# Performance work log

Measured on AMD Instinct MI355X. Metric: run time of the kernel, lower is better.

Reference implementation:

```python
import jax, jax.numpy as jnp
import numpy as np

N = 50000      # nodes
E = 800000     # edges (before self-loops)
IN = 128       # in_dim
OUT = 128      # out_dim
H = 4          # heads
C = OUT // H   # per-head channels
G = 64         # number of graphs in batch
NEG_SLOPE = 0.2
GN_EPS = 1e-5


def setup_inputs() -> dict:
    key = jax.random.key(0)
    ks = jax.random.split(key, 6)
    x = jax.random.normal(ks[0], (N, IN), dtype=jnp.float32)
    edge_index = jax.random.randint(ks[1], (2, E), 0, N, dtype=jnp.int32)
    batch = jnp.sort(jax.random.randint(ks[2], (N,), 0, G, dtype=jnp.int32))
    # glorot-ish init for GATv2 params
    s = float(np.sqrt(6.0 / (IN + H * C)))
    Wl = jax.random.uniform(ks[3], (IN, H * C), jnp.float32, -s, s)  # source (lin_l)
    Wr = jax.random.uniform(ks[4], (IN, H * C), jnp.float32, -s, s)  # target (lin_r)
    sa = float(np.sqrt(6.0 / (C + 1)))
    att = jax.random.uniform(ks[5], (H, C), jnp.float32, -sa, sa)
    bias_conv = jnp.zeros((H * C,), jnp.float32)
    gn_weight = jnp.ones((OUT,), jnp.float32)
    gn_bias = jnp.zeros((OUT,), jnp.float32)
    gn_mean_scale = jnp.ones((OUT,), jnp.float32)
    return {"x": x, "edge_index": edge_index, "batch": batch,
            "Wl": Wl, "Wr": Wr, "att": att, "bias_conv": bias_conv,
            "gn_weight": gn_weight, "gn_bias": gn_bias, "gn_mean_scale": gn_mean_scale}


def reference(x, edge_index, batch, Wl, Wr, att, bias_conv, gn_weight, gn_bias, gn_mean_scale):
    n = x.shape[0]
    # --- GATv2Conv (eval: dropout off), add_self_loops=True ---
    loop = jnp.arange(n, dtype=edge_index.dtype)
    src = jnp.concatenate([edge_index[0], loop])  # source j
    dst = jnp.concatenate([edge_index[1], loop])  # target i
    xl = (x @ Wl).reshape(n, H, C)  # source-side features
    xr = (x @ Wr).reshape(n, H, C)  # target-side features
    m = xl[src] + xr[dst]                               # [E', H, C]
    e = jax.nn.leaky_relu(m, NEG_SLOPE)
    logits = jnp.einsum('ehc,hc->eh', e, att)           # [E', H]
    # segment softmax over destination nodes
    amax = jax.ops.segment_max(logits, dst, num_segments=n)   # [N, H]
    ex = jnp.exp(logits - amax[dst])
    denom = jax.ops.segment_sum(ex, dst, num_segments=n)      # [N, H]
    alpha = ex / (denom[dst] + 1e-16)
    out = jax.ops.segment_sum(alpha[:, :, None] * xl[src], dst, num_segments=n)  # [N, H, C]
    out = out.reshape(n, H * C) + bias_conv
    # --- GraphNorm: (x - a*mean_g) / sqrt(var_g + eps) * w + b ---
    ones = jnp.ones((n, 1), out.dtype)
    cnt = jnp.maximum(jax.ops.segment_sum(ones, batch, num_segments=G), 1.0)  # [G, 1]
    mean = jax.ops.segment_sum(out, batch, num_segments=G) / cnt             # [G, OUT]
    out_c = out - mean[batch] * gn_mean_scale
    var = jax.ops.segment_sum(out_c * out_c, batch, num_segments=G) / cnt    # [G, OUT]
    y = out_c / jnp.sqrt(var[batch] + GN_EPS) * gn_weight + gn_bias
    # --- ELU ---
    return jax.nn.elu(y)
```

## Files before the change

### kernel.cpp

```cpp
#include <hip/hip_runtime.h>
#include <math.h>

#define HH 4
#define GG 64
#define CHUNK 64
#define BDST 16
#define BSH  4
#define SLOT 768
#define NPT  16
#define HWORDS 3328
constexpr float NEG_SLOPE = 0.2f;
constexpr float GN_EPS = 1e-5f;

typedef __attribute__((ext_vector_type(8))) short bf16x8;
typedef __attribute__((ext_vector_type(4))) float f32x4;

__device__ __forceinline__ unsigned short f2bf_rne(float f) {
  unsigned u = __float_as_uint(f);
  u += 0x7fffu + ((u >> 16) & 1u);
  return (unsigned short)(u >> 16);
}

__global__ __launch_bounds__(256) void wpack(
    const float* __restrict__ Wl, const float* __restrict__ Wr,
    unsigned short* __restrict__ Bfrag) {
  int tid = blockIdx.x * 256 + threadIdx.x;
  int f = tid >> 6, l = tid & 63;
  int m = f >> 5;
  int t = (f >> 2) & 7;
  int ks = f & 3;
  int col = t * 16 + (l & 15);
  int k0 = ks * 32 + (l >> 4) * 8;
  const float* W = m ? Wr : Wl;
  unsigned short* dst = Bfrag + ((size_t)f * 64 + l) * 8;
  #pragma unroll
  for (int j = 0; j < 8; ++j)
    dst[j] = f2bf_rne(W[(k0 + j) * 128 + col]);
}

__global__ __launch_bounds__(256) void gemm_mfma(
    const float* __restrict__ x, const unsigned short* __restrict__ Bfrag,
    unsigned short* __restrict__ xlb, float* __restrict__ xr, int n) {
  const int wave = (blockIdx.x * 256 + threadIdx.x) >> 6;
  if (wave * 16 >= n) return;
  const int l = threadIdx.x & 63;
  const int arow = min(wave * 16 + (l & 15), n - 1);
  const float4* xrow = reinterpret_cast<const float4*>(x + (size_t)arow * 128);

  bf16x8 a[4];
  #pragma unroll
  for (int ks = 0; ks < 4; ++ks) {
    float4 lo = xrow[ks * 8 + (l >> 4) * 2];
    float4 hi = xrow[ks * 8 + (l >> 4) * 2 + 1];
    bf16x8 v;
    v[0] = (short)f2bf_rne(lo.x); v[1] = (short)f2bf_rne(lo.y);
    v[2] = (short)f2bf_rne(lo.z); v[3] = (short)f2bf_rne(lo.w);
    v[4] = (short)f2bf_rne(hi.x); v[5] = (short)f2bf_rne(hi.y);
    v[6] = (short)f2bf_rne(hi.z); v[7] = (short)f2bf_rne(hi.w);
    a[ks] = v;
  }

  const int r0 = wave * 16 + (l >> 4) * 4;
  const int cb = l & 15;
  #pragma unroll
  for (int t = 0; t < 8; ++t) {
    f32x4 acc = {0.f, 0.f, 0.f, 0.f};
    #pragma unroll
    for (int ks = 0; ks < 4; ++ks) {
      const bf16x8* bp = reinterpret_cast<const bf16x8*>(
          Bfrag + ((size_t)((0 * 8 + t) * 4 + ks) * 64 + l) * 8);
      acc = __builtin_amdgcn_mfma_f32_16x16x32_bf16(a[ks], *bp, acc, 0, 0, 0);
    }
    #pragma unroll
    for (int j = 0; j < 4; ++j) {
      int r = r0 + j;
      if (r < n) xlb[(size_t)r * 128 + t * 16 + cb] = f2bf_rne(acc[j]);
    }
  }
  #pragma unroll
  for (int t = 0; t < 8; ++t) {
    f32x4 acc = {0.f, 0.f, 0.f, 0.f};
    #pragma unroll
    for (int ks = 0; ks < 4; ++ks) {
      const bf16x8* bp = reinterpret_cast<const bf16x8*>(
          Bfrag + ((size_t)((1 * 8 + t) * 4 + ks) * 64 + l) * 8);
      acc = __builtin_amdgcn_mfma_f32_16x16x32_bf16(a[ks], *bp, acc, 0, 0, 0);
    }
    #pragma unroll
    for (int j = 0; j < 4; ++j) {
      int r = r0 + j;
      if (r < n) xr[(size_t)r * 128 + t * 16 + cb] = acc[j];
    }
  }
}

__global__ __launch_bounds__(256) void bucket_scatter(
    const int* __restrict__ ei, int* __restrict__ gcur,
    int* __restrict__ ebuf, int E, int E2, int nbk) {
  __shared__ int hist[HWORDS];
  const int t = threadIdx.x;
  for (int i = t; i < HWORDS; i += 256) hist[i] = 0;
  __syncthreads();
  unsigned wcache[NPT];
  const int base = blockIdx.x * (256 * NPT);
  #pragma unroll
  for (int i = 0; i < NPT; ++i) {
    int e = base + i * 256 + t;
    unsigned w = 0xFFFFFFFFu;
    if (e < E2) {
      int src, dst;
      if (e < E) { src = ei[e]; dst = ei[E + e]; }
      else       { src = e - E; dst = e - E; }
      w = ((unsigned)(dst >> BSH) << 20) | ((unsigned)(dst & (BDST - 1)) << 16)
          | (unsigned)src;
      atomicAdd(&hist[dst >> BSH], 1);
    }
    wcache[i] = w;
  }
  __syncthreads();
  for (int b = t; b < nbk; b += 256) {
    int c = hist[b];
    if (c) hist[b] = atomicAdd(&gcur[b], c);
  }
  __syncthreads();
  #pragma unroll
  for (int i = 0; i < NPT; ++i) {
    unsigned w = wcache[i];
    if (w == 0xFFFFFFFFu) continue;
    int b = w >> 20;
    int pos = atomicAdd(&hist[b], 1);
    if (pos < SLOT) ebuf[b * SLOT + pos] = (int)(w & 0xFFFFF);
  }
}

__global__ __launch_bounds__(256) void fused_aggr(
    const int* __restrict__ gcur, const int* __restrict__ ebuf,
    const unsigned char* __restrict__ xb,
    const float* __restrict__ xr, const float* __restrict__ att,
    float* __restrict__ out, int n) {
  __shared__ int eraw[SLOT];
  __shared__ int elist[SLOT + 16];
  __shared__ int ldeg[BDST];
  __shared__ int lrow[BDST + 1];
  __shared__ int lcur[BDST];
  const int b = blockIdx.x;
  const int t = threadIdx.x;
  const int cnt = min(gcur[b], SLOT);
  if (t < BDST) ldeg[t] = 0;
  __syncthreads();
  for (int i = t; i < cnt; i += 256) {
    int w = ebuf[b * SLOT + i];
    eraw[i] = w;
    atomicAdd(&ldeg[(w >> 16) & (BDST - 1)], 1);
  }
  __syncthreads();
  if (t < BDST) {
    int v = ldeg[t];
    int incl = v;
    #pragma unroll
    for (int d = 1; d < BDST; d <<= 1) {
      int u = __shfl_up(incl, d);
      if (t >= d) incl += u;
    }
    lrow[t] = incl - v;
    lcur[t] = incl - v;
    if (t == BDST - 1) lrow[BDST] = incl;
  }
  __syncthreads();
  for (int i = t; i < cnt; i += 256) {
    int w = eraw[i];
    int pos = atomicAdd(&lcur[(w >> 16) & (BDST - 1)], 1);
    elist[pos] = (w & 0xFFFF) << 8;
  }
  if (t < 16) elist[cnt + t] = 0;
  __syncthreads();

  const int wv = t >> 6, lane = t & 63;
  const int q = lane & 31, hf = lane >> 5;
  const float4 at4 = *reinterpret_cast<const float4*>(att + q * 4);

  #define LDE(st) (*reinterpret_cast<const uint2*>( \
      xb + (size_t)(unsigned)ep[2 * (st) + hf] + q * 8))
  #define STEP(V, ebase) { \
    float x0 = __uint_as_float((V).x << 16); \
    float x1 = __uint_as_float((V).x & 0xffff0000u); \
    float x2 = __uint_as_float((V).y << 16); \
    float x3 = __uint_as_float((V).y & 0xffff0000u); \
    float t0 = x0 + xr4.x; t0 = fmaxf(t0, NEG_SLOPE * t0); \
    float t1 = x1 + xr4.y; t1 = fmaxf(t1, NEG_SLOPE * t1); \
    float t2 = x2 + xr4.z; t2 = fmaxf(t2, NEG_SLOPE * t2); \
    float t3 = x3 + xr4.w; t3 = fmaxf(t3, NEG_SLOPE * t3); \
    float p = fmaf(t3, at4.w, fmaf(t2, at4.z, fmaf(t1, at4.y, t0 * at4.x))); \
    p += __shfl_xor(p, 1); \
    p += __shfl_xor(p, 2); \
    p += __shfl_xor(p, 4); \
    float w = ((ebase) + hf < deg) ? __expf(p) : 0.f; \
    s += w; \
    a0 = fmaf(w, x0, a0); a1 = fmaf(w, x1, a1); \
    a2 = fmaf(w, x2, a2); a3 = fmaf(w, x3, a3); }

  for (int j = 0; j < 4; ++j) {
    const int ldst = wv * 4 + j;
    const int node = b * BDST + ldst;
    if (node >= n) break;
    const float4 xr4 = *reinterpret_cast<const float4*>(xr + (size_t)node * 128 + q * 4);
    const int k0 = lrow[ldst];
    const int deg = lrow[ldst + 1] - k0;
    const int* ep = elist + k0;

    uint2 V0 = LDE(0), V1 = LDE(1), V2 = LDE(2), V3 = LDE(3);
    float s = 0.f, a0 = 0.f, a1 = 0.f, a2 = 0.f, a3 = 0.f;
    const int S = (deg + 1) >> 1;
    for (int i = 0; i < S; i += 2) {
      STEP(V0, 2 * i)
      STEP(V1, 2 * i + 2)
      V0 = V2; V1 = V3;
      if (2 * i + 8 < deg)  V2 = LDE(i + 4);
      if (2 * i + 10 < deg) V3 = LDE(i + 5);
    }
    s  += __shfl_xor(s, 32);
    a0 += __shfl_xor(a0, 32);
    a1 += __shfl_xor(a1, 32);
    a2 += __shfl_xor(a2, 32);
    a3 += __shfl_xor(a3, 32);
    float inv = 1.f / (s + 1e-16f);
    if (hf == 0)
      *reinterpret_cast<float4*>(out + (size_t)node * 128 + q * 4) =
          make_float4(a0 * inv, a1 * inv, a2 * inv, a3 * inv);
  }
  #undef STEP
  #undef LDE
}

__global__ __launch_bounds__(128) void gn_stats(
    const float* __restrict__ out, const float* __restrict__ bias,
    const int* __restrict__ batch, float* __restrict__ gsum,
    float* __restrict__ gsumsq, int* __restrict__ gcnt, int n) {
  const int c = threadIdx.x;
  const int n0 = blockIdx.x * CHUNK;
  const int n1 = min(n0 + CHUNK, n);
  const float bc = bias[c];
  float bsum = 0.f, bsq = 0.f;
  int cnt = 0;
  int curg = batch[n0];
  for (int nid = n0; nid < n1; ++nid) {
    int g = batch[nid];
    if (g != curg) {
      atomicAdd(&gsum[curg * 128 + c], bsum);
      atomicAdd(&gsumsq[curg * 128 + c], bsq);
      if (c == 0) atomicAdd(&gcnt[curg], cnt);
      bsum = 0.f; bsq = 0.f; cnt = 0; curg = g;
    }
    float v = out[(size_t)nid * 128 + c] + bc;
    bsum += v; bsq += v * v; ++cnt;
  }
  atomicAdd(&gsum[curg * 128 + c], bsum);
  atomicAdd(&gsumsq[curg * 128 + c], bsq);
  if (c == 0) atomicAdd(&gcnt[curg], cnt);
}

__global__ __launch_bounds__(128) void gn_prep(
    const float* __restrict__ gsum, const float* __restrict__ gsumsq,
    const int* __restrict__ gcnt, const float* __restrict__ bias,
    const float* __restrict__ msc, const float* __restrict__ w,
    const float* __restrict__ b, float* __restrict__ K, float* __restrict__ S) {
  int g = blockIdx.x, c = threadIdx.x;
  float cnt = (float)max(gcnt[g], 1);
  float mean = gsum[g * 128 + c] / cnt;
  float a = msc[c];
  float var = gsumsq[g * 128 + c] / cnt - mean * mean * (2.f * a - a * a);
  float k = rsqrtf(var + GN_EPS) * w[c];
  K[g * 128 + c] = k;
  S[g * 128 + c] = (bias[c] - mean * a) * k + b[c];
}

__global__ __launch_bounds__(256) void gn_norm(
    float* __restrict__ out, const int* __restrict__ batch,
    const float* __restrict__ K, const float* __restrict__ S, int n) {
  long long i = (long long)blockIdx.x * 256 + threadIdx.x;
  if (i >= (long long)n * 128) return;
  int nid = (int)(i >> 7), c = (int)(i & 127);
  int g = batch[nid];
  float val = fmaf(out[i], K[g * 128 + c], S[g * 128 + c]);
  out[i] = (val > 0.f) ? val : (__expf(val) - 1.f);
}

extern "C" void kernel_launch(void* const* d_in, const int* in_sizes, int n_in,
                              void* d_out, int out_size, void* d_ws, size_t ws_size,
                              hipStream_t stream) {
  const float* x    = (const float*)d_in[0];
  const int*   ei   = (const int*)d_in[1];
  const int*   batch= (const int*)d_in[2];
  const float* Wl   = (const float*)d_in[3];
  const float* Wr   = (const float*)d_in[4];
  const float* att  = (const float*)d_in[5];
  const float* bias = (const float*)d_in[6];
  const float* gw   = (const float*)d_in[7];
  const float* gb   = (const float*)d_in[8];
  const float* gms  = (const float*)d_in[9];
  float* out = (float*)d_out;

  const int n  = in_sizes[0] / 128;
  const int E  = in_sizes[1] / 2;
  const int E2 = E + n;
  const int NBK = (n + BDST - 1) / BDST;

  char* ws = (char*)d_ws;
  size_t off = 0;
  int*   gcur    = (int*)(ws + off); off += (size_t)((NBK + 63) & ~63) * 4;
  int*   gcnt    = (int*)(ws + off); off += GG * 4;
  float* gsum    = (float*)(ws + off); off += GG * 128 * 4;
  float* gsumsq  = (float*)(ws + off); off += GG * 128 * 4;
  size_t zero_bytes = off;
  int*   ebuf    = (int*)(ws + off); off += (size_t)NBK * SLOT * 4;
  unsigned short* xlb = (unsigned short*)(ws + off); off += (size_t)n * 128 * 2;
  float* xr      = (float*)(ws + off); off += (size_t)n * 128 * 4;
  unsigned short* Bfrag = (unsigned short*)(ws + off); off += 64 * 64 * 8 * 2;
  float* gK      = (float*)(ws + off); off += GG * 128 * 4;
  float* gS      = (float*)(ws + off); off += GG * 128 * 4;

  hipMemsetAsync(ws, 0, zero_bytes, stream);

  bucket_scatter<<<(E2 + 256 * NPT - 1) / (256 * NPT), 256, 0, stream>>>(
      ei, gcur, ebuf, E, E2, NBK);

  wpack<<<16, 256, 0, stream>>>(Wl, Wr, (unsigned short*)Bfrag);
  {
    int waves = (n + 15) / 16;
    int blocks = (waves * 64 + 255) / 256;
    gemm_mfma<<<blocks, 256, 0, stream>>>(x, Bfrag, xlb, xr, n);
  }

  fused_aggr<<<NBK, 256, 0, stream>>>(gcur, ebuf, (const unsigned char*)xlb,
                                      xr, att, out, n);

  gn_stats<<<(n + CHUNK - 1) / CHUNK, 128, 0, stream>>>(out, bias, batch, gsum, gsumsq, gcnt, n);
  gn_prep<<<GG, 128, 0, stream>>>(gsum, gsumsq, gcnt, bias, gms, gw, gb, gK, gS);

  long long t_nm = (long long)n * 128;
  gn_norm<<<(int)((t_nm + 255) / 256), 256, 0, stream>>>(out, batch, gK, gS, n);
}
```

Before: 130.8 us.

## Merge bucket scatter with GEMM, widen aggregation lanes, vectorize GraphNorm apply

Merges the edge bucket-scatter kernel and the MFMA projection GEMM into one launch, with blocks split by index, so the two independent phases share a grid and one launch is dropped. The aggregation kernel now has each lane handle 8 channels (16-byte loads) and processes 4 edges per wave step instead of 2. The per-head reduction needs fewer shuffles, but more registers are held per lane. The GraphNorm apply kernel now uses float4 loads and stores. The merged kernel's blocks all reserve the histogram shared memory, including the GEMM blocks, which may lower their occupancy.

New measurement: 116.9 us. 1.12x faster.

```diff
diff --git a/kernel.cpp b/kernel.cpp
--- a/kernel.cpp
+++ b/kernel.cpp
@@ -38,12 +38,51 @@
     dst[j] = f2bf_rne(W[(k0 + j) * 128 + col]);
 }
 
-__global__ __launch_bounds__(256) void gemm_mfma(
+__global__ __launch_bounds__(256) void prep_merged(
+    const int* __restrict__ ei, int* __restrict__ gcur, int* __restrict__ ebuf,
+    int E, int E2, int nbk, int SB,
     const float* __restrict__ x, const unsigned short* __restrict__ Bfrag,
     unsigned short* __restrict__ xlb, float* __restrict__ xr, int n) {
-  const int wave = (blockIdx.x * 256 + threadIdx.x) >> 6;
+  __shared__ int hist[HWORDS];
+  const int t = threadIdx.x;
+  if ((int)blockIdx.x < SB) {
+    for (int i = t; i < HWORDS; i += 256) hist[i] = 0;
+    __syncthreads();
+    unsigned wcache[NPT];
+    const int base = blockIdx.x * (256 * NPT);
+    #pragma unroll
+    for (int i = 0; i < NPT; ++i) {
+      int e = base + i * 256 + t;
+      unsigned w = 0xFFFFFFFFu;
+      if (e < E2) {
+        int src, dst;
+        if (e < E) { src = ei[e]; dst = ei[E + e]; }
+        else       { src = e - E; dst = e - E; }
+        w = ((unsigned)(dst >> BSH) << 20) | ((unsigned)(dst & (BDST - 1)) << 16)
+            | (unsigned)src;
+        atomicAdd(&hist[dst >> BSH], 1);
+      }
+      wcache[i] = w;
+    }
+    __syncthreads();
+    for (int b = t; b < nbk; b += 256) {
+      int c = hist[b];
+      if (c) hist[b] = atomicAdd(&gcur[b], c);
+    }
+    __syncthreads();
+    #pragma unroll
+    for (int i = 0; i < NPT; ++i) {
+      unsigned w = wcache[i];
+      if (w == 0xFFFFFFFFu) continue;
+      int b = w >> 20;
+      int pos = atomicAdd(&hist[b], 1);
+      if (pos < SLOT) ebuf[b * SLOT + pos] = (int)(w & 0xFFFFF);
+    }
+    return;
+  }
+  const int wave = ((blockIdx.x - SB) * 256 + t) >> 6;
   if (wave * 16 >= n) return;
-  const int l = threadIdx.x & 63;
+  const int l = t & 63;
   const int arow = min(wave * 16 + (l & 15), n - 1);
   const float4* xrow = reinterpret_cast<const float4*>(x + (size_t)arow * 128);
 
@@ -63,73 +102,34 @@
   const int r0 = wave * 16 + (l >> 4) * 4;
   const int cb = l & 15;
   #pragma unroll
-  for (int t = 0; t < 8; ++t) {
+  for (int tt = 0; tt < 8; ++tt) {
     f32x4 acc = {0.f, 0.f, 0.f, 0.f};
     #pragma unroll
     for (int ks = 0; ks < 4; ++ks) {
       const bf16x8* bp = reinterpret_cast<const bf16x8*>(
-          Bfrag + ((size_t)((0 * 8 + t) * 4 + ks) * 64 + l) * 8);
+          Bfrag + ((size_t)((0 * 8 + tt) * 4 + ks) * 64 + l) * 8);
       acc = __builtin_amdgcn_mfma_f32_16x16x32_bf16(a[ks], *bp, acc, 0, 0, 0);
     }
     #pragma unroll
     for (int j = 0; j < 4; ++j) {
       int r = r0 + j;
-      if (r < n) xlb[(size_t)r * 128 + t * 16 + cb] = f2bf_rne(acc[j]);
+      if (r < n) xlb[(size_t)r * 128 + tt * 16 + cb] = f2bf_rne(acc[j]);
     }
   }
   #pragma unroll
-  for (int t = 0; t < 8; ++t) {
+  for (int tt = 0; tt < 8; ++tt) {
     f32x4 acc = {0.f, 0.f, 0.f, 0.f};
     #pragma unroll
     for (int ks = 0; ks < 4; ++ks) {
       const bf16x8* bp = reinterpret_cast<const bf16x8*>(
-          Bfrag + ((size_t)((1 * 8 + t) * 4 + ks) * 64 + l) * 8);
+          Bfrag + ((size_t)((1 * 8 + tt) * 4 + ks) * 64 + l) * 8);
       acc = __builtin_amdgcn_mfma_f32_16x16x32_bf16(a[ks], *bp, acc, 0, 0, 0);
     }
     #pragma unroll
     for (int j = 0; j < 4; ++j) {
       int r = r0 + j;
-      if (r < n) xr[(size_t)r * 128 + t * 16 + cb] = acc[j];
-    }
-  }
-}
-
-__global__ __launch_bounds__(256) void bucket_scatter(
-    const int* __restrict__ ei, int* __restrict__ gcur,
-    int* __restrict__ ebuf, int E, int E2, int nbk) {
-  __shared__ int hist[HWORDS];
-  const int t = threadIdx.x;
-  for (int i = t; i < HWORDS; i += 256) hist[i] = 0;
-  __syncthreads();
-  unsigned wcache[NPT];
-  const int base = blockIdx.x * (256 * NPT);
-  #pragma unroll
-  for (int i = 0; i < NPT; ++i) {
-    int e = base + i * 256 + t;
-    unsigned w = 0xFFFFFFFFu;
-    if (e < E2) {
-      int src, dst;
-      if (e < E) { src = ei[e]; dst = ei[E + e]; }
-      else       { src = e - E; dst = e - E; }
-      w = ((unsigned)(dst >> BSH) << 20) | ((unsigned)(dst & (BDST - 1)) << 16)
-          | (unsigned)src;
-      atomicAdd(&hist[dst >> BSH], 1);
-    }
-    wcache[i] = w;
-  }
-  __syncthreads();
-  for (int b = t; b < nbk; b += 256) {
-    int c = hist[b];
-    if (c) hist[b] = atomicAdd(&gcur[b], c);
-  }
-  __syncthreads();
-  #pragma unroll
-  for (int i = 0; i < NPT; ++i) {
-    unsigned w = wcache[i];
-    if (w == 0xFFFFFFFFu) continue;
-    int b = w >> 20;
-    int pos = atomicAdd(&hist[b], 1);
-    if (pos < SLOT) ebuf[b * SLOT + pos] = (int)(w & 0xFFFFF);
+      if (r < n) xr[(size_t)r * 128 + tt * 16 + cb] = acc[j];
+    }
   }
 }
 
@@ -176,57 +176,79 @@
   __syncthreads();
 
   const int wv = t >> 6, lane = t & 63;
-  const int q = lane & 31, hf = lane >> 5;
-  const float4 at4 = *reinterpret_cast<const float4*>(att + q * 4);
-
-  #define LDE(st) (*reinterpret_cast<const uint2*>( \
-      xb + (size_t)(unsigned)ep[2 * (st) + hf] + q * 8))
+  const int u = lane & 15, gi = lane >> 4;
+  const float4 atA = *reinterpret_cast<const float4*>(att + u * 8);
+  const float4 atB = *reinterpret_cast<const float4*>(att + u * 8 + 4);
+
+  #define LDE(st) (*reinterpret_cast<const uint4*>( \
+      xb + (size_t)(unsigned)ep[4 * (st) + gi] + u * 16))
   #define STEP(V, ebase) { \
     float x0 = __uint_as_float((V).x << 16); \
     float x1 = __uint_as_float((V).x & 0xffff0000u); \
     float x2 = __uint_as_float((V).y << 16); \
     float x3 = __uint_as_float((V).y & 0xffff0000u); \
-    float t0 = x0 + xr4.x; t0 = fmaxf(t0, NEG_SLOPE * t0); \
-    float t1 = x1 + xr4.y; t1 = fmaxf(t1, NEG_SLOPE * t1); \
-    float t2 = x2 + xr4.z; t2 = fmaxf(t2, NEG_SLOPE * t2); \
-    float t3 = x3 + xr4.w; t3 = fmaxf(t3, NEG_SLOPE * t3); \
-    float p = fmaf(t3, at4.w, fmaf(t2, at4.z, fmaf(t1, at4.y, t0 * at4.x))); \
+    float x4 = __uint_as_float((V).z << 16); \
+    float x5 = __uint_as_float((V).z & 0xffff0000u); \
+    float x6 = __uint_as_float((V).w << 16); \
+    float x7 = __uint_as_float((V).w & 0xffff0000u); \
+    float t0 = x0 + xrA.x; t0 = fmaxf(t0, NEG_SLOPE * t0); \
+    float t1 = x1 + xrA.y; t1 = fmaxf(t1, NEG_SLOPE * t1); \
+    float t2 = x2 + xrA.z; t2 = fmaxf(t2, NEG_SLOPE * t2); \
+    float t3 = x3 + xrA.w; t3 = fmaxf(t3, NEG_SLOPE * t3); \
+    float t4 = x4 + xrB.x; t4 = fmaxf(t4, NEG_SLOPE * t4); \
+    float t5 = x5 + xrB.y; t5 = fmaxf(t5, NEG_SLOPE * t5); \
+    float t6 = x6 + xrB.z; t6 = fmaxf(t6, NEG_SLOPE * t6); \
+    float t7 = x7 + xrB.w; t7 = fmaxf(t7, NEG_SLOPE * t7); \
+    float p = t0 * atA.x; \
+    p = fmaf(t1, atA.y, p); p = fmaf(t2, atA.z, p); p = fmaf(t3, atA.w, p); \
+    p = fmaf(t4, atB.x, p); p = fmaf(t5, atB.y, p); p = fmaf(t6, atB.z, p); \
+    p = fmaf(t7, atB.w, p); \
     p += __shfl_xor(p, 1); \
     p += __shfl_xor(p, 2); \
-    p += __shfl_xor(p, 4); \
-    float w = ((ebase) + hf < deg) ? __expf(p) : 0.f; \
+    float w = ((ebase) + gi < deg) ? __expf(p) : 0.f; \
     s += w; \
     a0 = fmaf(w, x0, a0); a1 = fmaf(w, x1, a1); \
-    a2 = fmaf(w, x2, a2); a3 = fmaf(w, x3, a3); }
+    a2 = fmaf(w, x2, a2); a3 = fmaf(w, x3, a3); \
+    a4 = fmaf(w, x4, a4); a5 = fmaf(w, x5, a5); \
+    a6 = fmaf(w, x6, a6); a7 = fmaf(w, x7, a7); }
 
   for (int j = 0; j < 4; ++j) {
     const int ldst = wv * 4 + j;
     const int node = b * BDST + ldst;
     if (node >= n) break;
-    const float4 xr4 = *reinterpret_cast<const float4*>(xr + (size_t)node * 128 + q * 4);
+    const float4 xrA = *reinterpret_cast<const float4*>(xr + (size_t)node * 128 + u * 8);
+    const float4 xrB = *reinterpret_cast<const float4*>(xr + (size_t)node * 128 + u * 8 + 4);
     const int k0 = lrow[ldst];
     const int deg = lrow[ldst + 1] - k0;
     const int* ep = elist + k0;
 
-    uint2 V0 = LDE(0), V1 = LDE(1), V2 = LDE(2), V3 = LDE(3);
-    float s = 0.f, a0 = 0.f, a1 = 0.f, a2 = 0.f, a3 = 0.f;
-    const int S = (deg + 1) >> 1;
-    for (int i = 0; i < S; i += 2) {
-      STEP(V0, 2 * i)
-      STEP(V1, 2 * i + 2)
-      V0 = V2; V1 = V3;
-      if (2 * i + 8 < deg)  V2 = LDE(i + 4);
-      if (2 * i + 10 < deg) V3 = LDE(i + 5);
-    }
-    s  += __shfl_xor(s, 32);
-    a0 += __shfl_xor(a0, 32);
-    a1 += __shfl_xor(a1, 32);
-    a2 += __shfl_xor(a2, 32);
-    a3 += __shfl_xor(a3, 32);
+    uint4 V0 = LDE(0), V1 = LDE(1), V2 = LDE(2);
+    float s = 0.f;
+    float a0 = 0.f, a1 = 0.f, a2 = 0.f, a3 = 0.f;
+    float a4 = 0.f, a5 = 0.f, a6 = 0.f, a7 = 0.f;
+    const int S = (deg + 3) >> 2;
+    for (int i = 0; i < S; ++i) {
+      uint4 C = V0; V0 = V1; V1 = V2;
+      if (4 * i + 12 < deg) V2 = LDE(i + 3);
+      STEP(C, 4 * i)
+    }
+    s  += __shfl_xor(s, 16);  s  += __shfl_xor(s, 32);
+    a0 += __shfl_xor(a0, 16); a0 += __shfl_xor(a0, 32);
+    a1 += __shfl_xor(a1, 16); a1 += __shfl_xor(a1, 32);
+    a2 += __shfl_xor(a2, 16); a2 += __shfl_xor(a2, 32);
+    a3 += __shfl_xor(a3, 16); a3 += __shfl_xor(a3, 32);
+    a4 += __shfl_xor(a4, 16); a4 += __shfl_xor(a4, 32);
+    a5 += __shfl_xor(a5, 16); a5 += __shfl_xor(a5, 32);
+    a6 += __shfl_xor(a6, 16); a6 += __shfl_xor(a6, 32);
+    a7 += __shfl_xor(a7, 16); a7 += __shfl_xor(a7, 32);
     float inv = 1.f / (s + 1e-16f);
-    if (hf == 0)
-      *reinterpret_cast<float4*>(out + (size_t)node * 128 + q * 4) =
+    if (gi == 0) {
+      float* op = out + (size_t)node * 128 + u * 8;
+      *reinterpret_cast<float4*>(op) =
           make_float4(a0 * inv, a1 * inv, a2 * inv, a3 * inv);
+      *reinterpret_cast<float4*>(op + 4) =
+          make_float4(a4 * inv, a5 * inv, a6 * inv, a7 * inv);
+    }
   }
   #undef STEP
   #undef LDE
@@ -277,12 +299,19 @@
 __global__ __launch_bounds__(256) void gn_norm(
     float* __restrict__ out, const int* __restrict__ batch,
     const float* __restrict__ K, const float* __restrict__ S, int n) {
-  long long i = (long long)blockIdx.x * 256 + threadIdx.x;
-  if (i >= (long long)n * 128) return;
-  int nid = (int)(i >> 7), c = (int)(i & 127);
+  int i = blockIdx.x * 256 + threadIdx.x;
+  if (i >= n * 32) return;
+  int nid = i >> 5, c4 = (i & 31) * 4;
   int g = batch[nid];
-  float val = fmaf(out[i], K[g * 128 + c], S[g * 128 + c]);
-  out[i] = (val > 0.f) ? val : (__expf(val) - 1.f);
+  const float4 k4 = *reinterpret_cast<const float4*>(K + g * 128 + c4);
+  const float4 s4 = *reinterpret_cast<const float4*>(S + g * 128 + c4);
+  float* op = out + (size_t)nid * 128 + c4;
+  float4 v = *reinterpret_cast<const float4*>(op);
+  v.x = fmaf(v.x, k4.x, s4.x); v.x = (v.x > 0.f) ? v.x : (__expf(v.x) - 1.f);
+  v.y = fmaf(v.y, k4.y, s4.y); v.y = (v.y > 0.f) ? v.y : (__expf(v.y) - 1.f);
+  v.z = fmaf(v.z, k4.z, s4.z); v.z = (v.z > 0.f) ? v.z : (__expf(v.z) - 1.f);
+  v.w = fmaf(v.w, k4.w, s4.w); v.w = (v.w > 0.f) ? v.w : (__expf(v.w) - 1.f);
+  *reinterpret_cast<float4*>(op) = v;
 }
 
 extern "C" void kernel_launch(void* const* d_in, const int* in_sizes, int n_in,
@@ -304,6 +333,8 @@
   const int E  = in_sizes[1] / 2;
   const int E2 = E + n;
   const int NBK = (n + BDST - 1) / BDST;
+  const int SB = (E2 + 256 * NPT - 1) / (256 * NPT);
+  const int GB = (((n + 15) / 16) * 64 + 255) / 256;
 
   char* ws = (char*)d_ws;
   size_t off = 0;
@@ -321,15 +352,10 @@
 
   hipMemsetAsync(ws, 0, zero_bytes, stream);
 
-  bucket_scatter<<<(E2 + 256 * NPT - 1) / (256 * NPT), 256, 0, stream>>>(
-      ei, gcur, ebuf, E, E2, NBK);
-
   wpack<<<16, 256, 0, stream>>>(Wl, Wr, (unsigned short*)Bfrag);
-  {
-    int waves = (n + 15) / 16;
-    int blocks = (waves * 64 + 255) / 256;
-    gemm_mfma<<<blocks, 256, 0, stream>>>(x, Bfrag, xlb, xr, n);
-  }
+
+  prep_merged<<<SB + GB, 256, 0, stream>>>(ei, gcur, ebuf, E, E2, NBK, SB,
+                                           x, Bfrag, xlb, xr, n);
 
   fused_aggr<<<NBK, 256, 0, stream>>>(gcur, ebuf, (const unsigned char*)xlb,
                                       xr, att, out, n);
@@ -337,6 +363,5 @@
   gn_stats<<<(n + CHUNK - 1) / CHUNK, 128, 0, stream>>>(out, bias, batch, gsum, gsumsq, gcnt, n);
   gn_prep<<<GG, 128, 0, stream>>>(gsum, gsumsq, gcnt, bias, gms, gw, gb, gK, gS);
 
-  long long t_nm = (long long)n * 128;
-  gn_norm<<<(int)((t_nm + 255) / 256), 256, 0, stream>>>(out, batch, gK, gS, n);
-}
+  gn_norm<<<(n * 32 + 255) / 256, 256, 0, stream>>>(out, batch, gK, gS, n);
+}
```
